# Performance work log

Hardware: AMD Instinct MI355X
Metric: run time of the kernel (lower is better)

Reference implementation:

```python
import jax, jax.numpy as jnp
import numpy as np

A = -0.75  # PyTorch bicubic coefficient
NEG_SLOPE = 0.01  # LeakyReLU default


def _cubic_kernel(s):
    # s: absolute distance, PyTorch cubic convolution kernel with a=-0.75
    s = jnp.abs(s)
    w1 = ((A + 2.0) * s - (A + 3.0)) * s * s + 1.0          # |s| <= 1
    w2 = (((s - 5.0) * s + 8.0) * s - 4.0) * A               # 1 < |s| < 2
    return jnp.where(s <= 1.0, w1, jnp.where(s < 2.0, w2, 0.0))


def _resize_matrix(n_in, n_out):
    """[n_out, n_in] bicubic interpolation matrix, align_corners=True, border-clamped."""
    scale = (n_in - 1) / (n_out - 1)
    src = jnp.arange(n_out, dtype=jnp.float32) * jnp.float32(scale)
    i0 = jnp.floor(src).astype(jnp.int32)
    t = src - i0.astype(jnp.float32)
    offs = jnp.arange(-1, 3)                     # [-1, 0, 1, 2]
    idx = jnp.clip(i0[:, None] + offs[None, :], 0, n_in - 1)   # [n_out, 4]
    w = _cubic_kernel(t[:, None] - offs[None, :].astype(jnp.float32))  # [n_out, 4]
    rows = jnp.broadcast_to(jnp.arange(n_out)[:, None], idx.shape)
    return jnp.zeros((n_out, n_in), dtype=jnp.float32).at[rows, idx].add(w)


def setup_inputs() -> dict:
    key = jax.random.key(0)
    k1, k2, k3 = jax.random.split(key, 3)
    B, C_IN, C_OUT, H, W = 8, 256, 128, 128, 128
    x = jax.random.normal(k1, (B, C_IN, H, W), dtype=jnp.float32)
    weight = jax.random.normal(k2, (C_OUT, C_IN), dtype=jnp.float32) * (1.0 / np.sqrt(C_IN))
    bias = jax.random.normal(k3, (C_OUT,), dtype=jnp.float32) * 0.01
    return {"x": x, "weight": weight, "bias": bias}


def reference(x, weight, bias):
    B, C, H, W = x.shape
    Mh = _resize_matrix(H, 2 * H)   # [2H, H]
    Mw = _resize_matrix(W, 2 * W)   # [2W, W]
    # Separable bicubic upsample: up[b,c,i,j] = sum_hw Mh[i,h] x[b,c,h,w] Mw[j,w]
    up = jnp.einsum('ih,bchw,jw->bcij', Mh, x, Mw)
    # 1x1 conv (per-pixel channel matmul) + bias
    y = jnp.einsum('oc,bcij->boij', weight, up) + bias[None, :, None, None]
    # LeakyReLU(0.01)
    return jnp.where(y >= 0, y, NEG_SLOPE * y)
```

## Files before the change

kernel.cpp:

```cpp
#include <hip/hip_runtime.h>
#include <hip/hip_bf16.h>

#define BB 8
#define CIN 256
#define COUT 128
#define HIN 128
#define WIN 128
#define HOUT 256
#define WOUT 256

typedef __attribute__((ext_vector_type(8))) short bf16x8;
typedef __attribute__((ext_vector_type(4))) float f32x4;

__device__ __forceinline__ short f2bf(float f) {
  __hip_bfloat16 h = __float2bfloat16(f);
  return *reinterpret_cast<short*>(&h);
}
__device__ __forceinline__ float bf2f(short s) {
  unsigned int u = ((unsigned int)(unsigned short)s) << 16;
  return __uint_as_float(u);
}

typedef __attribute__((address_space(3))) unsigned int lds_u32;
typedef const __attribute__((address_space(1))) unsigned int glb_u32;
__device__ __forceinline__ void gload16(const float* g, float* l) {
  __builtin_amdgcn_global_load_lds((glb_u32*)g, (lds_u32*)l, 16, 0, 0);
}

__global__ __launch_bounds__(256) void wconv_kernel(const float* __restrict__ wgt,
                                                    short* __restrict__ wbf) {
  int idx = (blockIdx.x * 256 + threadIdx.x) * 4;
  float4 f = *reinterpret_cast<const float4*>(wgt + idx);
  short4 pk = make_short4(f2bf(f.x), f2bf(f.y), f2bf(f.z), f2bf(f.w));
  *reinterpret_cast<short4*>(wbf + idx) = pk;
}

__global__ __launch_bounds__(256, 4) void conv1x1_kernel(const float* __restrict__ x,
                                                         const short* __restrict__ wbf,
                                                         short* __restrict__ zbf) {
  __shared__ __align__(16) float smemf[64 * 128];
  short* smems = (short*)smemf;
  const int h = blockIdx.x, b = blockIdx.y;
  const int t = threadIdx.x;
  const int lane = t & 63, wid = t >> 6;
  const int wm = wid >> 1, wn = wid & 1;
  const int r = lane & 15, g = lane >> 4;

  const float* xb = x + (size_t)b * (CIN * HIN * WIN) + (size_t)h * WIN;

  f32x4 acc[4][4];
#pragma unroll
  for (int i = 0; i < 4; ++i)
#pragma unroll
    for (int j = 0; j < 4; ++j)
      acc[i][j] = (f32x4){0.f, 0.f, 0.f, 0.f};

  const int lplane = lane >> 5;
  const int lw4 = (lane & 31) * 4;

  for (int ph = 0; ph < 4; ++ph) {
    const int cbase = ph * 64 + wid * 16;
#pragma unroll
    for (int i = 0; i < 8; ++i) {
      const float* src = xb + (size_t)(cbase + i * 2 + lplane) * (HIN * WIN) + lw4;
      float* dst = &smemf[(wid * 16 + i * 2) * 128];
      gload16(src, dst);
    }
    asm volatile("s_waitcnt vmcnt(0)" ::: "memory");
    __syncthreads();

#pragma unroll
    for (int ks = 0; ks < 2; ++ks) {
      const int cl0 = ks * 32 + g * 8;
      const int kg = ph * 8 + ks * 4 + g;
      bf16x8 xfr[4], wfr[4];
#pragma unroll
      for (int mt = 0; mt < 4; ++mt) {
        const int w = wm * 64 + mt * 16 + r;
#pragma unroll
        for (int j = 0; j < 8; ++j)
          xfr[mt][j] = f2bf(smemf[(cl0 + j) * 128 + w]);
      }
#pragma unroll
      for (int nt = 0; nt < 4; ++nt) {
        const int o = wn * 64 + nt * 16 + r;
        wfr[nt] = *reinterpret_cast<const bf16x8*>(wbf + (size_t)o * CIN + kg * 8);
      }
#pragma unroll
      for (int mt = 0; mt < 4; ++mt)
#pragma unroll
        for (int nt = 0; nt < 4; ++nt)
          acc[mt][nt] = __builtin_amdgcn_mfma_f32_16x16x32_bf16(xfr[mt], wfr[nt], acc[mt][nt], 0, 0, 0);
    }
    __syncthreads();
  }

#pragma unroll
  for (int mt = 0; mt < 4; ++mt) {
#pragma unroll
    for (int nt = 0; nt < 4; ++nt) {
      int o = wn * 64 + nt * 16 + r;
      int w4 = wm * 64 + mt * 16 + g * 4;
      int cw = w4 >> 3, sub = w4 & 7;
      short4 pk = make_short4(f2bf(acc[mt][nt][0]), f2bf(acc[mt][nt][1]),
                              f2bf(acc[mt][nt][2]), f2bf(acc[mt][nt][3]));
      *reinterpret_cast<short4*>(&smems[o * 128 + ((cw ^ (o & 15)) << 3) + sub]) = pk;
    }
  }
  __syncthreads();

  short* zb = zbf + (size_t)b * (COUT * HIN * WIN) + (size_t)h * WIN;
  const int ck = t & 15;
#pragma unroll
  for (int p = 0; p < 8; ++p) {
    int ro = p * 16 + (t >> 4);
    bf16x8 v = *reinterpret_cast<const bf16x8*>(&smems[ro * 128 + ((ck ^ (ro & 15)) << 3)]);
    *reinterpret_cast<bf16x8*>(zb + (size_t)ro * (HIN * WIN) + ck * 8) = v;
  }
}

#define ACF (-0.75f)
#define NEG 0.01f

__device__ __forceinline__ float cub_le1(float s) {
  return ((ACF + 2.0f) * s - (ACF + 3.0f)) * s * s + 1.0f;
}
__device__ __forceinline__ float cub_gt1(float s) {
  return (((s - 5.0f) * s + 8.0f) * s - 4.0f) * ACF;
}
__device__ __forceinline__ float4 mkw(float tt) {
  return make_float4(cub_gt1(1.0f + tt), cub_le1(tt), cub_le1(1.0f - tt), cub_gt1(2.0f - tt));
}

__global__ __launch_bounds__(256) void upsample_kernel(const short* __restrict__ zbf,
                                                       const float* __restrict__ bias,
                                                       float* __restrict__ out) {
  __shared__ float zrow[20][128];
  __shared__ float trow[20][256];

  const int bx = blockIdx.x;
  const int itile = bx & 7;
  const int o = bx >> 3;
  const int b = blockIdx.y;
  const int t = threadIdx.x;

  const int m0 = itile * 16;
  const int hmin = max(m0 - 2, 0);
  const int hmax = min(m0 + 15 + 2, HIN - 1);
  const int nh = hmax - hmin + 1;

  {
    const short* zb = zbf + ((size_t)b * COUT + o) * (HIN * WIN);
    for (int q = t; q < nh * 16; q += 256) {
      int hr = q >> 4, c8 = (q & 15) * 8;
      bf16x8 v = *reinterpret_cast<const bf16x8*>(zb + (size_t)(hmin + hr) * WIN + c8);
      float4 lo = make_float4(bf2f(v[0]), bf2f(v[1]), bf2f(v[2]), bf2f(v[3]));
      float4 hi = make_float4(bf2f(v[4]), bf2f(v[5]), bf2f(v[6]), bf2f(v[7]));
      *reinterpret_cast<float4*>(&zrow[hr][c8]) = lo;
      *reinterpret_cast<float4*>(&zrow[hr][c8 + 4]) = hi;
    }
  }
  __syncthreads();

  {
    const int u = t & 127;
    const int pr = t >> 7;
    const float uf = (float)u;
    const float4 wA = mkw((255.0f - uf) * (1.0f / 255.0f));
    const float4 wB = mkw((127.0f - uf) * (1.0f / 255.0f));
    const int i0c = max(u - 2, 0);
    const int i1c = max(u - 1, 0);
    const int i2c = u;
    const int i3c = min(u + 1, WIN - 1);
    const int i4c = min(u + 2, WIN - 1);
    for (int hr = pr; hr < nh; hr += 2) {
      float z0 = zrow[hr][i0c], z1 = zrow[hr][i1c], z2 = zrow[hr][i2c];
      float z3 = zrow[hr][i3c], z4 = zrow[hr][i4c];
      float oa = wA.x * z0 + wA.y * z1 + wA.z * z2 + wA.w * z3;
      float ob = wB.x * z1 + wB.y * z2 + wB.z * z3 + wB.w * z4;
      *reinterpret_cast<float2*>(&trow[hr][u * 2]) = make_float2(oa, ob);
    }
  }
  __syncthreads();

  const float bv = bias[o];
  const int j4 = t & 63;
  const int iw = t >> 6;
  float* obase = out + ((size_t)b * COUT + o) * (HOUT * WOUT);
  for (int mm = iw; mm < 16; mm += 4) {
    int m = m0 + mm;
    float mf = (float)m;
    float4 wA = mkw((255.0f - mf) * (1.0f / 255.0f));
    float4 wB = mkw((127.0f - mf) * (1.0f / 255.0f));
    int r0 = max(m - 2, 0) - hmin;
    int r1 = max(m - 1, 0) - hmin;
    int r2 = m - hmin;
    int r3 = min(m + 1, HIN - 1) - hmin;
    int r4 = min(m + 2, HIN - 1) - hmin;
    float4 t0 = *reinterpret_cast<const float4*>(&trow[r0][j4 * 4]);
    float4 t1 = *reinterpret_cast<const float4*>(&trow[r1][j4 * 4]);
    float4 t2 = *reinterpret_cast<const float4*>(&trow[r2][j4 * 4]);
    float4 t3 = *reinterpret_cast<const float4*>(&trow[r3][j4 * 4]);
    float4 t4 = *reinterpret_cast<const float4*>(&trow[r4][j4 * 4]);
    f32x4 rA, rB;
    rA.x = wA.x * t0.x + wA.y * t1.x + wA.z * t2.x + wA.w * t3.x + bv;
    rA.y = wA.x * t0.y + wA.y * t1.y + wA.z * t2.y + wA.w * t3.y + bv;
    rA.z = wA.x * t0.z + wA.y * t1.z + wA.z * t2.z + wA.w * t3.z + bv;
    rA.w = wA.x * t0.w + wA.y * t1.w + wA.z * t2.w + wA.w * t3.w + bv;
    rB.x = wB.x * t1.x + wB.y * t2.x + wB.z * t3.x + wB.w * t4.x + bv;
    rB.y = wB.x * t1.y + wB.y * t2.y + wB.z * t3.y + wB.w * t4.y + bv;
    rB.z = wB.x * t1.z + wB.y * t2.z + wB.z * t3.z + wB.w * t4.z + bv;
    rB.w = wB.x * t1.w + wB.y * t2.w + wB.z * t3.w + wB.w * t4.w + bv;
    rA.x = rA.x >= 0.f ? rA.x : rA.x * NEG;
    rA.y = rA.y >= 0.f ? rA.y : rA.y * NEG;
    rA.z = rA.z >= 0.f ? rA.z : rA.z * NEG;
    rA.w = rA.w >= 0.f ? rA.w : rA.w * NEG;
    rB.x = rB.x >= 0.f ? rB.x : rB.x * NEG;
    rB.y = rB.y >= 0.f ? rB.y : rB.y * NEG;
    rB.z = rB.z >= 0.f ? rB.z : rB.z * NEG;
    rB.w = rB.w >= 0.f ? rB.w : rB.w * NEG;
    int iA = itile * 32 + 2 * mm;
    __builtin_nontemporal_store(rA, reinterpret_cast<f32x4*>(obase + (size_t)iA * WOUT + j4 * 4));
    __builtin_nontemporal_store(rB, reinterpret_cast<f32x4*>(obase + (size_t)(iA + 1) * WOUT + j4 * 4));
  }
}

extern "C" void kernel_launch(void* const* d_in, const int* in_sizes, int n_in,
                              void* d_out, int out_size, void* d_ws, size_t ws_size,
                              hipStream_t stream) {
  const float* x = (const float*)d_in[0];
  const float* wgt = (const float*)d_in[1];
  const float* bias = (const float*)d_in[2];
  float* out = (float*)d_out;

  short* zbf = (short*)d_ws;
  short* wbf = (short*)((char*)d_ws + (size_t)BB * COUT * HIN * WIN * sizeof(short));

  wconv_kernel<<<dim3(COUT * CIN / (256 * 4)), 256, 0, stream>>>(wgt, wbf);
  conv1x1_kernel<<<dim3(HIN, BB), 256, 0, stream>>>(x, wbf, zbf);
  upsample_kernel<<<dim3(COUT * 8, BB), 256, 0, stream>>>(zbf, bias, out);
}
```

Before: 89.06 us.

## Double-buffer conv1x1 input staging to overlap global loads with MFMA

The channel loop of the 1x1 conv kernel becomes 8 stages of 32 channels, ping-ponging between two LDS halves and prefetching two stages ahead through direct global-to-LDS loads. Partial vmcnt waits replace the full drain, so loads for the next stage can be in flight while MFMAs run on the current one. This is meant to hide global memory latency in a bandwidth-bound stage. It adds more barriers per iteration, and the smaller stages may give less work per barrier.

```diff
diff --git a/kernel.cpp b/kernel.cpp
--- a/kernel.cpp
+++ b/kernel.cpp
@@ -38,7 +38,7 @@
 __global__ __launch_bounds__(256, 4) void conv1x1_kernel(const float* __restrict__ x,
                                                          const short* __restrict__ wbf,
                                                          short* __restrict__ zbf) {
-  __shared__ __align__(16) float smemf[64 * 128];
+  __shared__ __align__(16) float smemf[8192];
   short* smems = (short*)smemf;
   const int h = blockIdx.x, b = blockIdx.y;
   const int t = threadIdx.x;
@@ -47,6 +47,8 @@
   const int r = lane & 15, g = lane >> 4;
 
   const float* xb = x + (size_t)b * (CIN * HIN * WIN) + (size_t)h * WIN;
+  const int lplane = lane >> 5;
+  const int lw4 = (lane & 31) * 4;
 
   f32x4 acc[4][4];
 #pragma unroll
@@ -55,45 +57,57 @@
     for (int j = 0; j < 4; ++j)
       acc[i][j] = (f32x4){0.f, 0.f, 0.f, 0.f};
 
-  const int lplane = lane >> 5;
-  const int lw4 = (lane & 31) * 4;
-
-  for (int ph = 0; ph < 4; ++ph) {
-    const int cbase = ph * 64 + wid * 16;
-#pragma unroll
-    for (int i = 0; i < 8; ++i) {
-      const float* src = xb + (size_t)(cbase + i * 2 + lplane) * (HIN * WIN) + lw4;
-      float* dst = &smemf[(wid * 16 + i * 2) * 128];
-      gload16(src, dst);
-    }
-    asm volatile("s_waitcnt vmcnt(0)" ::: "memory");
-    __syncthreads();
-
-#pragma unroll
-    for (int ks = 0; ks < 2; ++ks) {
-      const int cl0 = ks * 32 + g * 8;
-      const int kg = ph * 8 + ks * 4 + g;
-      bf16x8 xfr[4], wfr[4];
-#pragma unroll
-      for (int mt = 0; mt < 4; ++mt) {
-        const int w = wm * 64 + mt * 16 + r;
-#pragma unroll
-        for (int j = 0; j < 8; ++j)
-          xfr[mt][j] = f2bf(smemf[(cl0 + j) * 128 + w]);
-      }
-#pragma unroll
-      for (int nt = 0; nt < 4; ++nt) {
-        const int o = wn * 64 + nt * 16 + r;
-        wfr[nt] = *reinterpret_cast<const bf16x8*>(wbf + (size_t)o * CIN + kg * 8);
-      }
-#pragma unroll
-      for (int mt = 0; mt < 4; ++mt)
-#pragma unroll
-        for (int nt = 0; nt < 4; ++nt)
-          acc[mt][nt] = __builtin_amdgcn_mfma_f32_16x16x32_bf16(xfr[mt], wfr[nt], acc[mt][nt], 0, 0, 0);
-    }
-    __syncthreads();
-  }
+#define STAGE(k)                                                               \
+  {                                                                            \
+    float* hbase = &smemf[((k) & 1) * 4096];                                   \
+    _Pragma("unroll") for (int i = 0; i < 4; ++i) {                            \
+      const float* src =                                                       \
+          xb + (size_t)((k) * 32 + wid * 8 + i * 2 + lplane) * (HIN * WIN) +   \
+          lw4;                                                                 \
+      gload16(src, &hbase[(wid * 8 + i * 2) * 128]);                           \
+    }                                                                          \
+  }
+
+  STAGE(0)
+  STAGE(1)
+
+#pragma unroll
+  for (int k = 0; k < 8; ++k) {
+    if (k < 7)
+      asm volatile("s_waitcnt vmcnt(4)" ::: "memory");
+    else
+      asm volatile("s_waitcnt vmcnt(0)" ::: "memory");
+    __builtin_amdgcn_s_barrier();
+
+    bf16x8 wfr[4];
+#pragma unroll
+    for (int nt = 0; nt < 4; ++nt) {
+      const int o = wn * 64 + nt * 16 + r;
+      wfr[nt] = *reinterpret_cast<const bf16x8*>(wbf + (size_t)o * CIN + (k * 4 + g) * 8);
+    }
+
+    const float* hb = &smemf[(k & 1) * 4096];
+    bf16x8 xfr[4];
+#pragma unroll
+    for (int mt = 0; mt < 4; ++mt) {
+      const int w = wm * 64 + mt * 16 + r;
+#pragma unroll
+      for (int j = 0; j < 8; ++j)
+        xfr[mt][j] = f2bf(hb[(g * 8 + j) * 128 + w]);
+    }
+#pragma unroll
+    for (int mt = 0; mt < 4; ++mt)
+#pragma unroll
+      for (int nt = 0; nt < 4; ++nt)
+        acc[mt][nt] = __builtin_amdgcn_mfma_f32_16x16x32_bf16(xfr[mt], wfr[nt], acc[mt][nt], 0, 0, 0);
+
+    asm volatile("s_waitcnt lgkmcnt(0)" ::: "memory");
+    __builtin_amdgcn_s_barrier();
+    if (k < 6) STAGE(k + 2)
+  }
+#undef STAGE
+
+  __syncthreads();
 
 #pragma unroll
   for (int mt = 0; mt < 4; ++mt) {
```

Result: slower. 91.22 us (+2.4%).
